# Optimization experiments

Measured on AMD Instinct MI355X. Metric: run time of the kernel, lower is better.

The kernel has to match this reference:

```python
import jax, jax.numpy as jnp
import numpy as np

B, S, H = 32, 1024, 512  # batch, src_len, hidden_dim


def setup_inputs() -> dict:
    key = jax.random.key(0)
    k1, k2, k3, k4, k5 = jax.random.split(key, 5)
    hidden = jax.random.normal(k1, (B, H), dtype=jnp.float32)
    encoder_outputs = jax.random.normal(k2, (B, S, 2 * H), dtype=jnp.float32)
    # nn.Linear(3H, H): weight stored here as [3H, H] (input-major) with bias [H]
    W = jax.random.normal(k3, (3 * H, H), dtype=jnp.float32) / np.sqrt(3 * H)
    b = jax.random.normal(k4, (H,), dtype=jnp.float32) * 0.01
    v = jax.random.normal(k5, (H,), dtype=jnp.float32) / np.sqrt(H)
    return {"hidden": hidden, "encoder_outputs": encoder_outputs, "W": W, "b": b, "v": v}


def reference(hidden, encoder_outputs, W, b, v):
    # concat((repeat(hidden), encoder_outputs)) @ W  ==  hidden @ W[:H] (broadcast) + enc @ W[H:]
    Wh, We = W[:H], W[H:]                         # [H,H], [2H,H]
    h_proj = hidden @ Wh                           # [B,H]
    e_proj = jnp.einsum('bse,eh->bsh', encoder_outputs, We)  # [B,S,H]
    energy = jnp.tanh(h_proj[:, None, :] + e_proj + b)       # [B,S,H]
    # bmm(v[B,1,H], energy^T[B,H,S]) -> scores [B,S]
    scores = jnp.einsum('bsh,h->bs', energy, v)
    return jax.nn.softmax(scores, axis=1)
```

## Files before the change

kernel.cpp:

```cpp
#include <hip/hip_runtime.h>
#include <math.h>

#define B_ 32
#define S_ 1024
#define H_ 512
#define K_ 1024
#define M_ (B_ * S_)

typedef __attribute__((ext_vector_type(8))) short bf16x8;
typedef __attribute__((ext_vector_type(16))) float f32x16;

__device__ __forceinline__ void split_bf16(float f, unsigned short& hi, unsigned short& lo) {
    unsigned u = __float_as_uint(f);
    unsigned r = u + 0x8000u;
    hi = (unsigned short)(r >> 16);
    float fh = __uint_as_float(r & 0xffff0000u);
    float res = f - fh;
    lo = (unsigned short)((__float_as_uint(res) + 0x8000u) >> 16);
}

__device__ __forceinline__ void split8_store(const float4& x, const float4& y,
                                             unsigned short* hiP, unsigned short* loP) {
    float f[8] = {x.x, x.y, x.z, x.w, y.x, y.y, y.z, y.w};
    unsigned hr[8], lr[8];
    #pragma unroll
    for (int i = 0; i < 8; ++i) {
        unsigned u = __float_as_uint(f[i]);
        unsigned r = u + 0x8000u;
        hr[i] = r;
        float fh = __uint_as_float(r & 0xffff0000u);
        lr[i] = __float_as_uint(f[i] - fh) + 0x8000u;
    }
    uint4 Hv, Lv;
    Hv.x = __builtin_amdgcn_perm(hr[1], hr[0], 0x07060302u);
    Hv.y = __builtin_amdgcn_perm(hr[3], hr[2], 0x07060302u);
    Hv.z = __builtin_amdgcn_perm(hr[5], hr[4], 0x07060302u);
    Hv.w = __builtin_amdgcn_perm(hr[7], hr[6], 0x07060302u);
    Lv.x = __builtin_amdgcn_perm(lr[1], lr[0], 0x07060302u);
    Lv.y = __builtin_amdgcn_perm(lr[3], lr[2], 0x07060302u);
    Lv.z = __builtin_amdgcn_perm(lr[5], lr[4], 0x07060302u);
    Lv.w = __builtin_amdgcn_perm(lr[7], lr[6], 0x07060302u);
    *reinterpret_cast<uint4*>(hiP) = Hv;
    *reinterpret_cast<uint4*>(loP) = Lv;
}

__device__ __forceinline__ float fast_tanh(float x) {
    float xc = fminf(fmaxf(x, -15.f), 15.f);
    float t = __expf(2.0f * xc);
    return (t - 1.0f) * __builtin_amdgcn_rcpf(t + 1.0f);
}

__device__ __forceinline__ void async_copy16(const void* g, void* l) {
    __builtin_amdgcn_global_load_lds(
        (const __attribute__((address_space(1))) void*)g,
        (__attribute__((address_space(3))) void*)l, 16, 0, 0);
}

__global__ __launch_bounds__(256) void prep_kernel(
    const float* __restrict__ hidden, const float* __restrict__ W,
    const float* __restrict__ bias, float* __restrict__ hb,
    unsigned short* __restrict__ Wh, unsigned short* __restrict__ Wl)
{
    __shared__ float red[4][64];
    __shared__ float t[32][33];
    const int bx = blockIdx.x;
    if (bx < 256) {
        const int tid = threadIdx.x;
        const int h0  = (bx & 7) * 64;
        const int b   = bx >> 3;
        const int h   = h0 + (tid & 63);
        const int ks  = tid >> 6;
        const float* hrow = hidden + b * H_;
        float acc = 0.f;
        #pragma unroll 8
        for (int k = ks * 128; k < ks * 128 + 128; ++k)
            acc = fmaf(hrow[k], W[(size_t)k * H_ + h], acc);
        red[ks][tid & 63] = acc;
        __syncthreads();
        if (tid < 64)
            hb[b * H_ + h0 + tid] = red[0][tid] + red[1][tid] + red[2][tid]
                                  + red[3][tid] + bias[h0 + tid];
    } else {
        const float* We = W + (size_t)H_ * H_;
        const int cx = bx - 256;
        const int k0 = (cx & 31) * 32, n0 = (cx >> 5) * 32;
        const int tx = threadIdx.x & 31, ty = threadIdx.x >> 5;
        #pragma unroll
        for (int j = 0; j < 4; ++j) {
            const int k = ty + 8 * j;
            t[k][tx] = We[(size_t)(k0 + k) * H_ + n0 + tx];
        }
        __syncthreads();
        #pragma unroll
        for (int j = 0; j < 4; ++j) {
            const int n    = ty + 8 * j;
            const int ncol = n0 + n;
            const int k    = k0 + tx;
            unsigned short hi, lo;
            split_bf16(t[tx][n], hi, lo);
            const int c     = ncol >> 5;
            const int tt    = k >> 4;
            const int lane_ = ((k >> 3) & 1) * 32 + (ncol & 31);
            const size_t s  = ((size_t)(c * 64 + tt) * 64 + lane_) * 8 + (k & 7);
            Wh[s] = hi;
            Wl[s] = lo;
        }
    }
}

__global__ __launch_bounds__(512, 2) void gemm_fused(
    const float* __restrict__ EO,
    const unsigned short* __restrict__ Bth,
    const unsigned short* __restrict__ Btl,
    const float* __restrict__ hb, const float* __restrict__ v,
    float* __restrict__ partial)
{
    __shared__ unsigned short ldsA[2][2][8192];
    __shared__ unsigned short ldsB[3][2][8192];

    const int tid  = threadIdx.x;
    const int bid  = blockIdx.x;
    const int jb   = bid >> 3;
    const int mt   = (bid & 7) * 16 + (jb >> 1);
    const int nt   = jb & 1;
    const int row0 = mt * 256;
    const int col0 = nt * 256;
    const int batch = row0 >> 10;

    const int lane   = tid & 63;
    const int wave   = tid >> 6;
    const int wm     = wave >> 2, wn = wave & 3;
    const int lane32 = lane & 31, kh = lane >> 5;

    size_t gA[2];
    int offAw[2];
    #pragma unroll
    for (int s = 0; s < 2; ++s) {
        const int seg = tid + 512 * s;
        const int m = seg >> 2, sg = seg & 3;
        gA[s]    = (size_t)(row0 + m) * K_ + sg * 8;
        offAw[s] = ((m >> 5) * 2 + (sg >> 1)) * 512
                 + ((sg & 1) * 32 + ((m & 31) ^ sg)) * 8;
    }
    const unsigned short* gBh = Bth + ((size_t)(nt * 8 + wave) * 32768 + lane * 8);
    const unsigned short* gBl = Btl + ((size_t)(nt * 8 + wave) * 32768 + lane * 8);
    const int offBw = wave * 1024;

    f32x16 acc[4][2];
    #pragma unroll
    for (int fi = 0; fi < 4; ++fi)
        #pragma unroll
        for (int fj = 0; fj < 2; ++fj)
            #pragma unroll
            for (int e = 0; e < 16; ++e)
                acc[fi][fj][e] = 0.f;

    float4 a0[2], a1[2];
    #pragma unroll
    for (int s = 0; s < 2; ++s) {
        a0[s] = *reinterpret_cast<const float4*>(EO + gA[s]);
        a1[s] = *reinterpret_cast<const float4*>(EO + gA[s] + 4);
    }
    #pragma unroll
    for (int s = 0; s < 2; ++s)
        split8_store(a0[s], a1[s], &ldsA[0][0][offAw[s]], &ldsA[0][1][offAw[s]]);
    #pragma unroll
    for (int ks = 0; ks < 2; ++ks) {
        async_copy16(gBh + (0 + ks) * 512, &ldsB[0][0][offBw + ks * 512]);
        async_copy16(gBl + (0 + ks) * 512, &ldsB[0][1][offBw + ks * 512]);
    }
    #pragma unroll
    for (int ks = 0; ks < 2; ++ks) {
        async_copy16(gBh + (2 + ks) * 512, &ldsB[1][0][offBw + ks * 512]);
        async_copy16(gBl + (2 + ks) * 512, &ldsB[1][1][offBw + ks * 512]);
    }
    asm volatile("s_waitcnt vmcnt(4) lgkmcnt(0)\n\ts_barrier" ::: "memory");

    int bc = 0;
    for (int j = 0; j < 32; ++j) {
        const int cur = j & 1, nxt = cur ^ 1;
        const int bn  = (bc >= 1) ? bc - 1 : 2;

        if (j < 31) {
            const int k0n = 32 * (j + 1);
            #pragma unroll
            for (int s = 0; s < 2; ++s) {
                a0[s] = *reinterpret_cast<const float4*>(EO + gA[s] + k0n);
                a1[s] = *reinterpret_cast<const float4*>(EO + gA[s] + k0n + 4);
            }
        }
        if (j < 30) {
            const int tnxt = 2 * (j + 2);
            #pragma unroll
            for (int ks = 0; ks < 2; ++ks) {
                async_copy16(gBh + (tnxt + ks) * 512, &ldsB[bn][0][offBw + ks * 512]);
                async_copy16(gBl + (tnxt + ks) * 512, &ldsB[bn][1][offBw + ks * 512]);
            }
        }

        __builtin_amdgcn_s_setprio(1);
        bf16x8 b_h[2][2], b_l[2][2];
        #pragma unroll
        for (int fj = 0; fj < 2; ++fj)
            #pragma unroll
            for (int ks = 0; ks < 2; ++ks) {
                const int baseB = ((wn * 2 + fj) * 2 + ks) * 512 + lane * 8;
                b_h[fj][ks] = *reinterpret_cast<const bf16x8*>(&ldsB[bc][0][baseB]);
                b_l[fj][ks] = *reinterpret_cast<const bf16x8*>(&ldsB[bc][1][baseB]);
            }
        #pragma unroll
        for (int fi = 0; fi < 4; ++fi) {
            bf16x8 a_h[2], a_l[2];
            #pragma unroll
            for (int ks = 0; ks < 2; ++ks) {
                const int baseA = ((wm * 4 + fi) * 2 + ks) * 512
                                + (kh * 32 + (lane32 ^ (2 * ks + kh))) * 8;
                a_h[ks] = *reinterpret_cast<const bf16x8*>(&ldsA[cur][0][baseA]);
                a_l[ks] = *reinterpret_cast<const bf16x8*>(&ldsA[cur][1][baseA]);
            }
            #pragma unroll
            for (int fj = 0; fj < 2; ++fj)
                #pragma unroll
                for (int ks = 0; ks < 2; ++ks) {
                    acc[fi][fj] = __builtin_amdgcn_mfma_f32_32x32x16_bf16(
                        a_h[ks], b_h[fj][ks], acc[fi][fj], 0, 0, 0);
                    acc[fi][fj] = __builtin_amdgcn_mfma_f32_32x32x16_bf16(
                        a_h[ks], b_l[fj][ks], acc[fi][fj], 0, 0, 0);
                    acc[fi][fj] = __builtin_amdgcn_mfma_f32_32x32x16_bf16(
                        a_l[ks], b_h[fj][ks], acc[fi][fj], 0, 0, 0);
                }
        }
        __builtin_amdgcn_s_setprio(0);

        if (j < 30) {
            #pragma unroll
            for (int s = 0; s < 2; ++s)
                split8_store(a0[s], a1[s],
                             &ldsA[nxt][0][offAw[s]], &ldsA[nxt][1][offAw[s]]);
            asm volatile("s_waitcnt vmcnt(4) lgkmcnt(0)\n\ts_barrier" ::: "memory");
        } else if (j == 30) {
            #pragma unroll
            for (int s = 0; s < 2; ++s)
                split8_store(a0[s], a1[s],
                             &ldsA[nxt][0][offAw[s]], &ldsA[nxt][1][offAw[s]]);
            asm volatile("s_waitcnt vmcnt(0) lgkmcnt(0)\n\ts_barrier" ::: "memory");
        }
        bc = (bc == 2) ? 0 : bc + 1;
    }

    const float* hb_row = hb + batch * H_;
    float hbv[2], vv[2];
    #pragma unroll
    for (int fj = 0; fj < 2; ++fj) {
        const int c = col0 + (wn * 2 + fj) * 32 + lane32;
        hbv[fj] = hb_row[c];
        vv[fj]  = v[c];
    }
    float* red = reinterpret_cast<float*>(&ldsA[0][0][0]);
    #pragma unroll
    for (int fi = 0; fi < 4; ++fi)
        #pragma unroll
        for (int r = 0; r < 16; ++r) {
            float rs = 0.f;
            #pragma unroll
            for (int fj = 0; fj < 2; ++fj)
                rs = fmaf(fast_tanh(acc[fi][fj][r] + hbv[fj]), vv[fj], rs);
            rs += __shfl_xor(rs, 1, 64);
            rs += __shfl_xor(rs, 2, 64);
            rs += __shfl_xor(rs, 4, 64);
            rs += __shfl_xor(rs, 8, 64);
            rs += __shfl_xor(rs, 16, 64);
            if (lane32 == 0) {
                const int row = wm * 128 + fi * 32 + (r & 3) + 8 * (r >> 2) + 4 * kh;
                red[row * 4 + wn] = rs;
            }
        }
    __syncthreads();
    if (tid < 256)
        partial[(size_t)nt * M_ + row0 + tid] =
            red[tid * 4] + red[tid * 4 + 1] + red[tid * 4 + 2] + red[tid * 4 + 3];
}

__global__ __launch_bounds__(256) void softmax_kernel(
    const float* __restrict__ partial, float* __restrict__ out)
{
    const int b = blockIdx.x;
    const int tid = threadIdx.x;
    float val[4];
    float lmax = -3.0e38f;
    #pragma unroll
    for (int q = 0; q < 4; ++q) {
        const int idx = b * S_ + tid + 256 * q;
        float sum = partial[idx] + partial[M_ + idx];
        val[q] = sum;
        lmax = fmaxf(lmax, sum);
    }
    #pragma unroll
    for (int off = 32; off > 0; off >>= 1)
        lmax = fmaxf(lmax, __shfl_down(lmax, off, 64));
    __shared__ float wmax[4];
    if ((tid & 63) == 0) wmax[tid >> 6] = lmax;
    __syncthreads();
    const float gmax = fmaxf(fmaxf(wmax[0], wmax[1]), fmaxf(wmax[2], wmax[3]));
    float lsum = 0.0f;
    #pragma unroll
    for (int q = 0; q < 4; ++q) {
        val[q] = expf(val[q] - gmax);
        lsum += val[q];
    }
    #pragma unroll
    for (int off = 32; off > 0; off >>= 1)
        lsum += __shfl_down(lsum, off, 64);
    __shared__ float wsum[4];
    if ((tid & 63) == 0) wsum[tid >> 6] = lsum;
    __syncthreads();
    const float inv = 1.0f / (wsum[0] + wsum[1] + wsum[2] + wsum[3]);
    #pragma unroll
    for (int q = 0; q < 4; ++q)
        out[b * S_ + tid + 256 * q] = val[q] * inv;
}

extern "C" void kernel_launch(void* const* d_in, const int* in_sizes, int n_in,
                              void* d_out, int out_size, void* d_ws, size_t ws_size,
                              hipStream_t stream) {
    const float* hidden = (const float*)d_in[0];
    const float* EO     = (const float*)d_in[1];
    const float* W      = (const float*)d_in[2];
    const float* bias   = (const float*)d_in[3];
    const float* v      = (const float*)d_in[4];
    float* out          = (float*)d_out;

    float* hb      = (float*)d_ws;
    float* partial = hb + B_ * H_;
    unsigned short* Wth = (unsigned short*)(partial + 4 * M_);
    unsigned short* Wtl = Wth + (size_t)H_ * K_;

    prep_kernel<<<768, 256, 0, stream>>>(hidden, W, bias, hb, Wth, Wtl);
    gemm_fused<<<dim3(256), 512, 0, stream>>>(EO, Wth, Wtl, hb, v, partial);
    softmax_kernel<<<B_, 256, 0, stream>>>(partial, out);
}
```

Baseline: 287.1 us.

## Split main loop into two barrier-separated MFMA phases interleaving loads

Each K iteration is split into two phases of half the M fragments each, in a ping-pong style. Global A loads, B async copies and the split-to-bf16 LDS stores are placed between phases so they overlap with the other waves' MFMA clusters. sched_barrier fences and explicit waitcnts keep the compiler from reordering across phases. This adds extra barriers per iteration, and a vmcnt wait at the end of each iteration that could stall, in exchange for better overlap of memory and matrix work.

```diff
diff --git a/kernel.cpp b/kernel.cpp
--- a/kernel.cpp
+++ b/kernel.cpp
@@ -162,9 +162,6 @@
         a1[s] = *reinterpret_cast<const float4*>(EO + gA[s] + 4);
     }
     #pragma unroll
-    for (int s = 0; s < 2; ++s)
-        split8_store(a0[s], a1[s], &ldsA[0][0][offAw[s]], &ldsA[0][1][offAw[s]]);
-    #pragma unroll
     for (int ks = 0; ks < 2; ++ks) {
         async_copy16(gBh + (0 + ks) * 512, &ldsB[0][0][offBw + ks * 512]);
         async_copy16(gBl + (0 + ks) * 512, &ldsB[0][1][offBw + ks * 512]);
@@ -174,31 +171,28 @@
         async_copy16(gBh + (2 + ks) * 512, &ldsB[1][0][offBw + ks * 512]);
         async_copy16(gBl + (2 + ks) * 512, &ldsB[1][1][offBw + ks * 512]);
     }
-    asm volatile("s_waitcnt vmcnt(4) lgkmcnt(0)\n\ts_barrier" ::: "memory");
+    #pragma unroll
+    for (int s = 0; s < 2; ++s)
+        split8_store(a0[s], a1[s], &ldsA[0][0][offAw[s]], &ldsA[0][1][offAw[s]]);
+    asm volatile("s_waitcnt vmcnt(4) lgkmcnt(0)" ::: "memory");
+    __builtin_amdgcn_s_barrier();
+
+#define PHASE_MFMA(fb)                                                         \
+    _Pragma("unroll") for (int ks = 0; ks < 2; ++ks)                           \
+      _Pragma("unroll") for (int p = 0; p < 3; ++p)                            \
+        _Pragma("unroll") for (int f2 = 0; f2 < 2; ++f2)                       \
+          _Pragma("unroll") for (int fj = 0; fj < 2; ++fj) {                   \
+            acc[(fb) + f2][fj] = __builtin_amdgcn_mfma_f32_32x32x16_bf16(      \
+                (p == 2) ? a_l[f2][ks] : a_h[f2][ks],                          \
+                (p == 1) ? b_l[fj][ks] : b_h[fj][ks],                          \
+                acc[(fb) + f2][fj], 0, 0, 0);                                  \
+          }
 
     int bc = 0;
     for (int j = 0; j < 32; ++j) {
         const int cur = j & 1, nxt = cur ^ 1;
         const int bn  = (bc >= 1) ? bc - 1 : 2;
 
-        if (j < 31) {
-            const int k0n = 32 * (j + 1);
-            #pragma unroll
-            for (int s = 0; s < 2; ++s) {
-                a0[s] = *reinterpret_cast<const float4*>(EO + gA[s] + k0n);
-                a1[s] = *reinterpret_cast<const float4*>(EO + gA[s] + k0n + 4);
-            }
-        }
-        if (j < 30) {
-            const int tnxt = 2 * (j + 2);
-            #pragma unroll
-            for (int ks = 0; ks < 2; ++ks) {
-                async_copy16(gBh + (tnxt + ks) * 512, &ldsB[bn][0][offBw + ks * 512]);
-                async_copy16(gBl + (tnxt + ks) * 512, &ldsB[bn][1][offBw + ks * 512]);
-            }
-        }
-
-        __builtin_amdgcn_s_setprio(1);
         bf16x8 b_h[2][2], b_l[2][2];
         #pragma unroll
         for (int fj = 0; fj < 2; ++fj)
@@ -208,45 +202,71 @@
                 b_h[fj][ks] = *reinterpret_cast<const bf16x8*>(&ldsB[bc][0][baseB]);
                 b_l[fj][ks] = *reinterpret_cast<const bf16x8*>(&ldsB[bc][1][baseB]);
             }
-        #pragma unroll
-        for (int fi = 0; fi < 4; ++fi) {
-            bf16x8 a_h[2], a_l[2];
-            #pragma unroll
-            for (int ks = 0; ks < 2; ++ks) {
-                const int baseA = ((wm * 4 + fi) * 2 + ks) * 512
-                                + (kh * 32 + (lane32 ^ (2 * ks + kh))) * 8;
-                a_h[ks] = *reinterpret_cast<const bf16x8*>(&ldsA[cur][0][baseA]);
-                a_l[ks] = *reinterpret_cast<const bf16x8*>(&ldsA[cur][1][baseA]);
-            }
-            #pragma unroll
-            for (int fj = 0; fj < 2; ++fj)
+        {
+            bf16x8 a_h[2][2], a_l[2][2];
+            #pragma unroll
+            for (int f2 = 0; f2 < 2; ++f2)
                 #pragma unroll
                 for (int ks = 0; ks < 2; ++ks) {
-                    acc[fi][fj] = __builtin_amdgcn_mfma_f32_32x32x16_bf16(
-                        a_h[ks], b_h[fj][ks], acc[fi][fj], 0, 0, 0);
-                    acc[fi][fj] = __builtin_amdgcn_mfma_f32_32x32x16_bf16(
-                        a_h[ks], b_l[fj][ks], acc[fi][fj], 0, 0, 0);
-                    acc[fi][fj] = __builtin_amdgcn_mfma_f32_32x32x16_bf16(
-                        a_l[ks], b_h[fj][ks], acc[fi][fj], 0, 0, 0);
+                    const int baseA = ((wm * 4 + f2) * 2 + ks) * 512
+                                    + (kh * 32 + (lane32 ^ (2 * ks + kh))) * 8;
+                    a_h[f2][ks] = *reinterpret_cast<const bf16x8*>(&ldsA[cur][0][baseA]);
+                    a_l[f2][ks] = *reinterpret_cast<const bf16x8*>(&ldsA[cur][1][baseA]);
                 }
-        }
-        __builtin_amdgcn_s_setprio(0);
-
-        if (j < 30) {
-            #pragma unroll
-            for (int s = 0; s < 2; ++s)
-                split8_store(a0[s], a1[s],
-                             &ldsA[nxt][0][offAw[s]], &ldsA[nxt][1][offAw[s]]);
-            asm volatile("s_waitcnt vmcnt(4) lgkmcnt(0)\n\ts_barrier" ::: "memory");
-        } else if (j == 30) {
-            #pragma unroll
-            for (int s = 0; s < 2; ++s)
-                split8_store(a0[s], a1[s],
-                             &ldsA[nxt][0][offAw[s]], &ldsA[nxt][1][offAw[s]]);
-            asm volatile("s_waitcnt vmcnt(0) lgkmcnt(0)\n\ts_barrier" ::: "memory");
+            if (j < 31) {
+                const int k0n = 32 * (j + 1);
+                #pragma unroll
+                for (int s = 0; s < 2; ++s) {
+                    a0[s] = *reinterpret_cast<const float4*>(EO + gA[s] + k0n);
+                    a1[s] = *reinterpret_cast<const float4*>(EO + gA[s] + k0n + 4);
+                }
+            }
+            __builtin_amdgcn_s_barrier();
+            asm volatile("s_waitcnt lgkmcnt(0)" ::: "memory");
+            __builtin_amdgcn_sched_barrier(0);
+            __builtin_amdgcn_s_setprio(1);
+            PHASE_MFMA(0)
+            __builtin_amdgcn_s_setprio(0);
+            __builtin_amdgcn_s_barrier();
+        }
+
+        {
+            bf16x8 a_h[2][2], a_l[2][2];
+            #pragma unroll
+            for (int f2 = 0; f2 < 2; ++f2)
+                #pragma unroll
+                for (int ks = 0; ks < 2; ++ks) {
+                    const int baseA = ((wm * 4 + 2 + f2) * 2 + ks) * 512
+                                    + (kh * 32 + (lane32 ^ (2 * ks + kh))) * 8;
+                    a_h[f2][ks] = *reinterpret_cast<const bf16x8*>(&ldsA[cur][0][baseA]);
+                    a_l[f2][ks] = *reinterpret_cast<const bf16x8*>(&ldsA[cur][1][baseA]);
+                }
+            if (j < 30) {
+                const int tnxt = 2 * (j + 2);
+                #pragma unroll
+                for (int ks = 0; ks < 2; ++ks) {
+                    async_copy16(gBh + (tnxt + ks) * 512, &ldsB[bn][0][offBw + ks * 512]);
+                    async_copy16(gBl + (tnxt + ks) * 512, &ldsB[bn][1][offBw + ks * 512]);
+                }
+            }
+            if (j < 31) {
+                #pragma unroll
+                for (int s = 0; s < 2; ++s)
+                    split8_store(a0[s], a1[s],
+                                 &ldsA[nxt][0][offAw[s]], &ldsA[nxt][1][offAw[s]]);
+            }
+            __builtin_amdgcn_s_barrier();
+            asm volatile("s_waitcnt lgkmcnt(0)" ::: "memory");
+            __builtin_amdgcn_sched_barrier(0);
+            __builtin_amdgcn_s_setprio(1);
+            PHASE_MFMA(2)
+            __builtin_amdgcn_s_setprio(0);
+            asm volatile("s_waitcnt vmcnt(4)" ::: "memory");
+            __builtin_amdgcn_s_barrier();
         }
         bc = (bc == 2) ? 0 : bc + 1;
     }
+#undef PHASE_MFMA
 
     const float* hb_row = hb + batch * H_;
     float hbv[2], vv[2];
```

New measurement: 292.5 us. No clear change (+1.9%).
